# Kernel tuning notes

Hardware: AMD Instinct MI355X
Metric: run time of the kernel (lower is better)

The kernel has to match this reference:

```python
import jax, jax.numpy as jnp
import numpy as np

B, S, D, H = 2, 2048, 1024, 16
DK = D // H


def setup_inputs() -> dict:
    key = jax.random.key(0)
    ks = jax.random.split(key, 12)
    scale = 1.0 / np.sqrt(D)
    inp = {
        "query": jax.random.normal(ks[0], (B, S, D), jnp.float32),
        "key_in": jax.random.normal(ks[1], (B, S, D), jnp.float32),
        "value": jax.random.normal(ks[2], (B, S, D), jnp.float32),
        "mask": jnp.ones((1, 1, S, S), dtype=bool),
        "w_q": jax.random.normal(ks[3], (D, D), jnp.float32) * scale,
        "b_q": jnp.zeros((D,), jnp.float32),
        "w_k": jax.random.normal(ks[4], (D, D), jnp.float32) * scale,
        "b_k": jnp.zeros((D,), jnp.float32),
        "w_v": jax.random.normal(ks[5], (D, D), jnp.float32) * scale,
        "b_v": jnp.zeros((D,), jnp.float32),
        "w_o": jax.random.normal(ks[6], (D, D), jnp.float32) * scale,
        "b_o": jnp.zeros((D,), jnp.float32),
    }
    return inp


def reference(query, key_in, value, mask, w_q, b_q, w_k, b_k, w_v, b_v, w_o, b_o):
    # QKV projections (nn.Linear: x @ W.T + b; here weights stored as [D_in, D_out])
    q = query @ w_q + b_q          # [B, S, D]
    k = key_in @ w_k + b_k
    v = value @ w_v + b_v
    # split heads -> [B, H, S, DK]
    q = q.reshape(B, S, H, DK).transpose(0, 2, 1, 3)
    k = k.reshape(B, S, H, DK).transpose(0, 2, 1, 3)
    v = v.reshape(B, S, H, DK).transpose(0, 2, 1, 3)
    # scaled dot-product attention (naive: full [B,H,S,S] scores)
    scores = jnp.einsum('bhqd,bhkd->bhqk', q, k) / jnp.sqrt(jnp.float32(DK))
    scores = jnp.where(mask, scores, jnp.float32(-1e9))
    probs = jax.nn.softmax(scores, axis=-1)  # dropout p=0.0 -> identity
    x = jnp.einsum('bhqk,bhkd->bhqd', probs, v)  # [B, H, S, DK]
    x = x.transpose(0, 2, 1, 3).reshape(B, S, D)
    return x @ w_o + b_o
```

## Files before the change

### kernel.cpp

```cpp
#include <hip/hip_runtime.h>
#include <cstdint>
#include <cstddef>


typedef _Float16 f16_t;
typedef _Float16 f16x8 __attribute__((ext_vector_type(8)));
typedef _Float16 f16x4 __attribute__((ext_vector_type(4)));
typedef float    f32x4 __attribute__((ext_vector_type(4)));

#define S_LEN 2048
#define DMODEL 1024
#define NHEAD 16
#define DK 64
#define NKV (S_LEN / 64)

__device__ __forceinline__ void async_copy16(void* lds, const void* g) {
    __builtin_amdgcn_global_load_lds(
        (const __attribute__((address_space(1))) unsigned int*)g,
        (__attribute__((address_space(3))) unsigned int*)lds,
        16, 0, 0);
}

__device__ __forceinline__ float fexp2(float x) {
#if __has_builtin(__builtin_amdgcn_exp2f)
    return __builtin_amdgcn_exp2f(x);
#else
    return exp2f(x);
#endif
}

__global__ __launch_bounds__(256) void cvt3_kernel(
    const float* __restrict__ s0, const float* __restrict__ s1, const float* __restrict__ s2,
    f16_t* __restrict__ d0, f16_t* __restrict__ d1, f16_t* __restrict__ d2, int n)
{
    const float* s = blockIdx.y == 0 ? s0 : blockIdx.y == 1 ? s1 : s2;
    f16_t*       d = blockIdx.y == 0 ? d0 : blockIdx.y == 1 ? d1 : d2;
    int i = (blockIdx.x * 256 + threadIdx.x) * 4;
    if (i + 3 < n) {
        f32x4 v = *(const f32x4*)(s + i);
        f16x4 o;
        o[0] = (f16_t)v[0]; o[1] = (f16_t)v[1];
        o[2] = (f16_t)v[2]; o[3] = (f16_t)v[3];
        *(f16x4*)(d + i) = o;
    }
}

__global__ __launch_bounds__(256) void transpose_cvt_kernel(
    const float* __restrict__ w0, const float* __restrict__ w1,
    const float* __restrict__ w2, const float* __restrict__ w3,
    f16_t* __restrict__ wt_base)
{
    __shared__ float tile[32][33];
    int z = blockIdx.z;
    const float* w = z == 0 ? w0 : z == 1 ? w1 : z == 2 ? w2 : w3;
    f16_t* wt = wt_base + (size_t)z * DMODEL * DMODEL;
    int tx = threadIdx.x, ty = threadIdx.y;
    int bx = blockIdx.x * 32;
    int by = blockIdx.y * 32;
#pragma unroll
    for (int i = 0; i < 4; ++i)
        tile[ty + i * 8][tx] = w[(size_t)(bx + ty + i * 8) * DMODEL + by + tx];
    __syncthreads();
#pragma unroll
    for (int i = 0; i < 4; ++i)
        wt[(size_t)(by + ty + i * 8) * DMODEL + bx + tx] = (f16_t)tile[tx][ty + i * 8];
}

__global__ __launch_bounds__(256) void qkv_gemm_kernel(
    const f16_t* __restrict__ Aq, const f16_t* __restrict__ Ak, const f16_t* __restrict__ Av,
    const f16_t* __restrict__ Bt,
    const float* __restrict__ bq, const float* __restrict__ bk, const float* __restrict__ bv,
    f16_t* __restrict__ q_h, f16_t* __restrict__ k_h, f16_t* __restrict__ v_t)
{
    __shared__ f16_t As[128 * 32];
    __shared__ f16_t Bs[128 * 32];

    int tid  = threadIdx.x;
    int lane = tid & 63;
    int w    = tid >> 6;
    int wm   = w >> 1, wn = w & 1;

    int lin = blockIdx.y * 24 + blockIdx.x;
    int swz = (lin & 7) * 96 + (lin >> 3);
    int bx  = swz % 24, by = swz / 24;
    int row0 = by * 128;
    int col0 = bx * 128;
    int which = col0 >> 10;
    const f16_t* A = which == 0 ? Aq : which == 1 ? Ak : Av;
    const float* bias = which == 0 ? bq : which == 1 ? bk : bv;

    f32x4 acc[4][4] = {};

    for (int kk = 0; kk < 1024; kk += 32) {
        __syncthreads();
#pragma unroll
        for (int j = 0; j < 2; ++j) {
            int c = w * 2 + j;
            int r = c * 16 + (lane >> 2);
            int e = (lane & 3) * 8;
            async_copy16(&As[c * 512], A  + (size_t)(row0 + r) * 1024 + kk + e);
            async_copy16(&Bs[c * 512], Bt + (size_t)(col0 + r) * 1024 + kk + e);
        }
        __syncthreads();

        f16x8 a[4], b[4];
#pragma unroll
        for (int mi = 0; mi < 4; ++mi)
            a[mi] = *(const f16x8*)&As[(wm * 64 + mi * 16 + (lane & 15)) * 32 + (lane >> 4) * 8];
#pragma unroll
        for (int ni = 0; ni < 4; ++ni)
            b[ni] = *(const f16x8*)&Bs[(wn * 64 + ni * 16 + (lane & 15)) * 32 + (lane >> 4) * 8];
#pragma unroll
        for (int mi = 0; mi < 4; ++mi)
#pragma unroll
            for (int ni = 0; ni < 4; ++ni)
                acc[mi][ni] = __builtin_amdgcn_mfma_f32_16x16x32_f16(a[mi], b[ni], acc[mi][ni], 0, 0, 0);
    }

    const float QSCALE = 0.125f * 1.4426950408889634f;
#pragma unroll
    for (int mi = 0; mi < 4; ++mi) {
#pragma unroll
        for (int ni = 0; ni < 4; ++ni) {
#pragma unroll
            for (int r = 0; r < 4; ++r) {
                int grow = row0 + wm * 64 + mi * 16 + (lane >> 4) * 4 + r;
                int gcol = col0 + wn * 64 + ni * 16 + (lane & 15);
                int nc   = gcol & 1023;
                float v  = acc[mi][ni][r] + bias[nc];
                int bb = grow >> 11, ss = grow & 2047;
                int hh = nc >> 6,    dd = nc & 63;
                if (which == 0)
                    q_h[(((size_t)(bb * NHEAD + hh) * S_LEN + ss) << 6) + dd] = (f16_t)(v * QSCALE);
                else if (which == 1)
                    k_h[(((size_t)(bb * NHEAD + hh) * S_LEN + ss) << 6) + dd] = (f16_t)v;
                else
                    v_t[((size_t)(bb * NHEAD + hh) * DK + dd) * S_LEN + ss] = (f16_t)v;
            }
        }
    }
}

__global__ __launch_bounds__(256) void out_gemm_kernel(
    const f16_t* __restrict__ A, const f16_t* __restrict__ Bt,
    const float* __restrict__ bias, float* __restrict__ outp)
{
    __shared__ f16_t As[128 * 32];
    __shared__ f16_t Bs[128 * 32];

    int tid  = threadIdx.x;
    int lane = tid & 63;
    int w    = tid >> 6;
    int wm   = w >> 1, wn = w & 1;

    int lin = blockIdx.y * 8 + blockIdx.x;
    int swz = (lin & 7) * 32 + (lin >> 3);
    int row0 = (swz / 8) * 128;
    int col0 = (swz % 8) * 128;

    f32x4 acc[4][4] = {};

    for (int kk = 0; kk < 1024; kk += 32) {
        __syncthreads();
#pragma unroll
        for (int j = 0; j < 2; ++j) {
            int c = w * 2 + j;
            int r = c * 16 + (lane >> 2);
            int e = (lane & 3) * 8;
            async_copy16(&As[c * 512], A  + (size_t)(row0 + r) * 1024 + kk + e);
            async_copy16(&Bs[c * 512], Bt + (size_t)(col0 + r) * 1024 + kk + e);
        }
        __syncthreads();

        f16x8 a[4], b[4];
#pragma unroll
        for (int mi = 0; mi < 4; ++mi)
            a[mi] = *(const f16x8*)&As[(wm * 64 + mi * 16 + (lane & 15)) * 32 + (lane >> 4) * 8];
#pragma unroll
        for (int ni = 0; ni < 4; ++ni)
            b[ni] = *(const f16x8*)&Bs[(wn * 64 + ni * 16 + (lane & 15)) * 32 + (lane >> 4) * 8];
#pragma unroll
        for (int mi = 0; mi < 4; ++mi)
#pragma unroll
            for (int ni = 0; ni < 4; ++ni)
                acc[mi][ni] = __builtin_amdgcn_mfma_f32_16x16x32_f16(a[mi], b[ni], acc[mi][ni], 0, 0, 0);
    }

#pragma unroll
    for (int mi = 0; mi < 4; ++mi)
#pragma unroll
        for (int ni = 0; ni < 4; ++ni)
#pragma unroll
            for (int r = 0; r < 4; ++r) {
                int grow = row0 + wm * 64 + mi * 16 + (lane >> 4) * 4 + r;
                int gcol = col0 + wn * 64 + ni * 16 + (lane & 15);
                outp[(size_t)grow * 1024 + gcol] = acc[mi][ni][r] + bias[gcol];
            }
}

__global__ __launch_bounds__(256) void flash_kernel(
    const f16_t* __restrict__ Q, const f16_t* __restrict__ K,
    const f16_t* __restrict__ Vt, f16_t* __restrict__ Ao)
{
    __shared__ f16_t Kl[2][64 * 64];
    __shared__ f16_t Vl[64 * 64];
    __shared__ f16_t Pw[4][16 * 72];

    int tid  = threadIdx.x;
    int lane = tid & 63;
    int li   = lane & 15;
    int g    = lane >> 4;
    int w    = tid >> 6;

    int lin = blockIdx.y * 32 + blockIdx.x;
    int swz = (lin & 7) * 128 + (lin >> 3);
    int qt  = swz & 31;
    int bh  = swz >> 5;

    const size_t hbase = (size_t)bh * S_LEN * DK;
    const f16_t* Qh = Q  + hbase;
    const f16_t* Kh = K  + hbase;
    const f16_t* Vh = Vt + hbase;

    int q0 = qt * 64 + w * 16;

    f16x8 aq[2];
#pragma unroll
    for (int kc = 0; kc < 2; ++kc)
        aq[kc] = *(const f16x8*)(Qh + (size_t)(q0 + li) * DK + kc * 32 + g * 8);

    f32x4 ot[4] = {};
    float mrun = -1e30f;
    float lrun = 0.f;

    auto stageV = [&](int kt) {
#pragma unroll
        for (int j = 0; j < 2; ++j) {
            int r0  = w * 16 + j * 8;
            int row = r0 + (lane >> 3);
            int sl  = (lane & 7) ^ (row & 7);
            async_copy16(&Vl[r0 * 64], Vh + (size_t)row * S_LEN + kt * 64 + sl * 8);
        }
    };
    auto stageK = [&](int buf, int kt) {
#pragma unroll
        for (int j = 0; j < 2; ++j) {
            int r0  = w * 16 + j * 8;
            int row = r0 + (lane >> 3);
            int sl  = (lane & 7) ^ (row & 7);
            async_copy16(&Kl[buf][r0 * 64], Kh + (size_t)(kt * 64 + row) * 64 + sl * 8);
        }
    };

    stageK(0, 0);
    int cur = 0;

    for (int kt = 0; kt < NKV; ++kt) {
        __syncthreads();
        stageV(kt);
        if (kt + 1 < NKV) stageK(cur ^ 1, kt + 1);

        f32x4 s[4] = {};
        __builtin_amdgcn_s_setprio(1);
#pragma unroll
        for (int kc = 0; kc < 2; ++kc)
#pragma unroll
            for (int kn = 0; kn < 4; ++kn) {
                int row = kn * 16 + li;
                int sp  = (kc * 4 + g) ^ (row & 7);
                f16x8 ak = *(const f16x8*)&Kl[cur][row * 64 + sp * 8];
                s[kn] = __builtin_amdgcn_mfma_f32_16x16x32_f16(ak, aq[kc], s[kn], 0, 0, 0);
            }
        __builtin_amdgcn_s_setprio(0);

        {
            float mx = fmaxf(fmaxf(fmaxf(s[0][0], s[0][1]), fmaxf(s[0][2], s[0][3])),
                             fmaxf(fmaxf(s[1][0], s[1][1]), fmaxf(s[1][2], s[1][3])));
            mx = fmaxf(mx, fmaxf(fmaxf(fmaxf(s[2][0], s[2][1]), fmaxf(s[2][2], s[2][3])),
                                 fmaxf(fmaxf(s[3][0], s[3][1]), fmaxf(s[3][2], s[3][3]))));
            mx = fmaxf(mx, __shfl_xor(mx, 16));
            mx = fmaxf(mx, __shfl_xor(mx, 32));
            if (!__all(mx - mrun <= 8.0f)) {
                float mn = fmaxf(mrun, mx);
                float alpha = fexp2(mrun - mn);
                mrun = mn;
                lrun *= alpha;
#pragma unroll
                for (int nd = 0; nd < 4; ++nd)
#pragma unroll
                    for (int r = 0; r < 4; ++r)
                        ot[nd][r] *= alpha;
            }
            float rs = 0.f;
#pragma unroll
            for (int kn = 0; kn < 4; ++kn) {
                f16x4 pv;
#pragma unroll
                for (int r = 0; r < 4; ++r) {
                    float p = fexp2(s[kn][r] - mrun);
                    rs += p;
                    pv[r] = (f16_t)p;
                }
                *(f16x4*)&Pw[w][li * 72 + kn * 16 + g * 4] = pv;
            }
            rs += __shfl_xor(rs, 16);
            rs += __shfl_xor(rs, 32);
            lrun += rs;
        }

        if (kt + 1 < NKV) asm volatile("s_waitcnt vmcnt(2)" ::: "memory");
        else              asm volatile("s_waitcnt vmcnt(0)" ::: "memory");

        __builtin_amdgcn_s_setprio(1);
#pragma unroll
        for (int kc = 0; kc < 2; ++kc) {
            f16x8 bp = *(const f16x8*)&Pw[w][li * 72 + kc * 32 + g * 8];
#pragma unroll
            for (int nd = 0; nd < 4; ++nd) {
                int row = nd * 16 + li;
                int sp  = (kc * 4 + g) ^ (row & 7);
                f16x8 av = *(const f16x8*)&Vl[row * 64 + sp * 8];
                ot[nd] = __builtin_amdgcn_mfma_f32_16x16x32_f16(av, bp, ot[nd], 0, 0, 0);
            }
        }
        __builtin_amdgcn_s_setprio(0);

        cur ^= 1;
    }

    int b = bh >> 4, h = bh & 15;
    {
        float inv = 1.0f / lrun;
        int qrow = q0 + li;
        size_t base = (size_t)(b * S_LEN + qrow) * DMODEL + h * 64;
#pragma unroll
        for (int nd = 0; nd < 4; ++nd) {
            f16x4 ov;
#pragma unroll
            for (int r = 0; r < 4; ++r)
                ov[r] = (f16_t)(ot[nd][r] * inv);
            *(f16x4*)&Ao[base + nd * 16 + g * 4] = ov;
        }
    }
}

extern "C" void kernel_launch(void* const* d_in, const int* in_sizes, int n_in,
                              void* d_out, int out_size, void* d_ws, size_t ws_size,
                              hipStream_t stream)
{
    const float* query  = (const float*)d_in[0];
    const float* key_in = (const float*)d_in[1];
    const float* value  = (const float*)d_in[2];
    const float* w_q = (const float*)d_in[4];
    const float* b_q = (const float*)d_in[5];
    const float* w_k = (const float*)d_in[6];
    const float* b_k = (const float*)d_in[7];
    const float* w_v = (const float*)d_in[8];
    const float* b_v = (const float*)d_in[9];
    const float* w_o = (const float*)d_in[10];
    const float* b_o = (const float*)d_in[11];
    float* out = (float*)d_out;

    char* ws = (char*)d_ws;
    const size_t MB = 1024 * 1024;
    f16_t* x_q  = (f16_t*)(ws + 0 * MB);
    f16_t* x_k  = (f16_t*)(ws + 8 * MB);
    f16_t* x_v  = (f16_t*)(ws + 16 * MB);
    f16_t* wt   = (f16_t*)(ws + 24 * MB);
    f16_t* wt_o = (f16_t*)(ws + 30 * MB);
    f16_t* q_h  = (f16_t*)(ws + 32 * MB);
    f16_t* k_h  = (f16_t*)(ws + 40 * MB);
    f16_t* v_t  = (f16_t*)(ws + 48 * MB);
    f16_t* attn = (f16_t*)(ws + 56 * MB);

    const int n = 2 * S_LEN * DMODEL;

    cvt3_kernel<<<dim3(n / 1024, 3), 256, 0, stream>>>(query, key_in, value, x_q, x_k, x_v, n);
    transpose_cvt_kernel<<<dim3(32, 32, 4), dim3(32, 8), 0, stream>>>(w_q, w_k, w_v, w_o, wt);

    qkv_gemm_kernel<<<dim3(24, 32), 256, 0, stream>>>(
        x_q, x_k, x_v, wt, b_q, b_k, b_v, q_h, k_h, v_t);

    flash_kernel<<<dim3(32, 32), 256, 0, stream>>>(q_h, k_h, v_t, attn);

    out_gemm_kernel<<<dim3(8, 32), 256, 0, stream>>>(attn, wt_o, b_o, out);
}
```

Measured before the change: 152.3 us.

## Compute softmax row sums via MFMA with ones, hoist LDS/global address math

The attention kernel now computes the softmax denominator with an extra MFMA that multiplies a ones vector by the f16 probability tile, instead of scalar sums plus cross-lane shuffles. It also precomputes swizzled LDS offsets and global source pointers outside the KV loop, and packs probabilities with the cvt_pkrtz instruction. The goal is to cut VALU and shuffle work in the softmax step and address arithmetic in the inner loop. In exchange it adds MFMA work, sums the f16-rounded probabilities rather than the fp32 values, and uses round-toward-zero conversion.

```diff
diff --git a/kernel.cpp b/kernel.cpp
--- a/kernel.cpp
+++ b/kernel.cpp
@@ -7,6 +7,7 @@
 typedef _Float16 f16x8 __attribute__((ext_vector_type(8)));
 typedef _Float16 f16x4 __attribute__((ext_vector_type(4)));
 typedef float    f32x4 __attribute__((ext_vector_type(4)));
+typedef unsigned int u32x2 __attribute__((ext_vector_type(2)));
 
 #define S_LEN 2048
 #define DMODEL 1024
@@ -26,6 +27,15 @@
     return __builtin_amdgcn_exp2f(x);
 #else
     return exp2f(x);
+#endif
+}
+
+__device__ __forceinline__ unsigned int cvt_pk_u32(float a, float b) {
+#if __has_builtin(__builtin_amdgcn_cvt_pkrtz)
+    return __builtin_bit_cast(unsigned int, __builtin_amdgcn_cvt_pkrtz(a, b));
+#else
+    union { f16_t h[2]; unsigned int u; } r;
+    r.h[0] = (f16_t)a; r.h[1] = (f16_t)b; return r.u;
 #endif
 }
 
@@ -229,28 +239,33 @@
     for (int kc = 0; kc < 2; ++kc)
         aq[kc] = *(const f16x8*)(Qh + (size_t)(q0 + li) * DK + kc * 32 + g * 8);
 
+    f16x8 ones;
+#pragma unroll
+    for (int i = 0; i < 8; ++i) ones[i] = (f16_t)1.0f;
+
     f32x4 ot[4] = {};
+    f32x4 lacc = {};
     float mrun = -1e30f;
-    float lrun = 0.f;
+
+    int lr  = lane >> 3;
+    int sl8 = ((lane & 7) ^ lr) * 8;
+    const f16_t* srcK = Kh + (size_t)(w * 16 + lr) * 64    + sl8;
+    const f16_t* srcV = Vh + (size_t)(w * 16 + lr) * S_LEN + sl8;
 
     auto stageV = [&](int kt) {
-#pragma unroll
-        for (int j = 0; j < 2; ++j) {
-            int r0  = w * 16 + j * 8;
-            int row = r0 + (lane >> 3);
-            int sl  = (lane & 7) ^ (row & 7);
-            async_copy16(&Vl[r0 * 64], Vh + (size_t)row * S_LEN + kt * 64 + sl * 8);
-        }
+        async_copy16(&Vl[(w * 16) * 64],     srcV + kt * 64);
+        async_copy16(&Vl[(w * 16 + 8) * 64], srcV + 8 * S_LEN + kt * 64);
     };
     auto stageK = [&](int buf, int kt) {
-#pragma unroll
-        for (int j = 0; j < 2; ++j) {
-            int r0  = w * 16 + j * 8;
-            int row = r0 + (lane >> 3);
-            int sl  = (lane & 7) ^ (row & 7);
-            async_copy16(&Kl[buf][r0 * 64], Kh + (size_t)(kt * 64 + row) * 64 + sl * 8);
-        }
+        const f16_t* p = srcK + (size_t)kt * 4096;
+        async_copy16(&Kl[buf][(w * 16) * 64],     p);
+        async_copy16(&Kl[buf][(w * 16 + 8) * 64], p + 512);
     };
+
+    int x0 = li * 64 + ((g    ) ^ (li & 7)) * 8;
+    int x1 = li * 64 + ((4 + g) ^ (li & 7)) * 8;
+    int pww = li * 72 + g * 4;
+    int pwr = li * 72 + g * 8;
 
     stageK(0, 0);
     int cur = 0;
@@ -266,46 +281,41 @@
         for (int kc = 0; kc < 2; ++kc)
 #pragma unroll
             for (int kn = 0; kn < 4; ++kn) {
-                int row = kn * 16 + li;
-                int sp  = (kc * 4 + g) ^ (row & 7);
-                f16x8 ak = *(const f16x8*)&Kl[cur][row * 64 + sp * 8];
+                f16x8 ak = *(const f16x8*)&Kl[cur][kn * 1024 + (kc ? x1 : x0)];
                 s[kn] = __builtin_amdgcn_mfma_f32_16x16x32_f16(ak, aq[kc], s[kn], 0, 0, 0);
             }
         __builtin_amdgcn_s_setprio(0);
 
         {
-            float mx = fmaxf(fmaxf(fmaxf(s[0][0], s[0][1]), fmaxf(s[0][2], s[0][3])),
-                             fmaxf(fmaxf(s[1][0], s[1][1]), fmaxf(s[1][2], s[1][3])));
-            mx = fmaxf(mx, fmaxf(fmaxf(fmaxf(s[2][0], s[2][1]), fmaxf(s[2][2], s[2][3])),
-                                 fmaxf(fmaxf(s[3][0], s[3][1]), fmaxf(s[3][2], s[3][3]))));
+            float mx = fmaxf(s[0][0], s[0][1]);
+            mx = fmaxf(fmaxf(mx, s[0][2]), s[0][3]);
+            mx = fmaxf(fmaxf(mx, s[1][0]), s[1][1]);
+            mx = fmaxf(fmaxf(mx, s[1][2]), s[1][3]);
+            mx = fmaxf(fmaxf(mx, s[2][0]), s[2][1]);
+            mx = fmaxf(fmaxf(mx, s[2][2]), s[2][3]);
+            mx = fmaxf(fmaxf(mx, s[3][0]), s[3][1]);
+            mx = fmaxf(fmaxf(mx, s[3][2]), s[3][3]);
             mx = fmaxf(mx, __shfl_xor(mx, 16));
             mx = fmaxf(mx, __shfl_xor(mx, 32));
             if (!__all(mx - mrun <= 8.0f)) {
                 float mn = fmaxf(mrun, mx);
                 float alpha = fexp2(mrun - mn);
                 mrun = mn;
-                lrun *= alpha;
+#pragma unroll
+                for (int r = 0; r < 4; ++r) lacc[r] *= alpha;
 #pragma unroll
                 for (int nd = 0; nd < 4; ++nd)
 #pragma unroll
                     for (int r = 0; r < 4; ++r)
                         ot[nd][r] *= alpha;
             }
-            float rs = 0.f;
 #pragma unroll
             for (int kn = 0; kn < 4; ++kn) {
-                f16x4 pv;
-#pragma unroll
-                for (int r = 0; r < 4; ++r) {
-                    float p = fexp2(s[kn][r] - mrun);
-                    rs += p;
-                    pv[r] = (f16_t)p;
-                }
-                *(f16x4*)&Pw[w][li * 72 + kn * 16 + g * 4] = pv;
-            }
-            rs += __shfl_xor(rs, 16);
-            rs += __shfl_xor(rs, 32);
-            lrun += rs;
+                u32x2 pv;
+                pv[0] = cvt_pk_u32(fexp2(s[kn][0] - mrun), fexp2(s[kn][1] - mrun));
+                pv[1] = cvt_pk_u32(fexp2(s[kn][2] - mrun), fexp2(s[kn][3] - mrun));
+                *(u32x2*)&Pw[w][pww + kn * 16] = pv;
+            }
         }
 
         if (kt + 1 < NKV) asm volatile("s_waitcnt vmcnt(2)" ::: "memory");
@@ -314,12 +324,11 @@
         __builtin_amdgcn_s_setprio(1);
 #pragma unroll
         for (int kc = 0; kc < 2; ++kc) {
-            f16x8 bp = *(const f16x8*)&Pw[w][li * 72 + kc * 32 + g * 8];
+            f16x8 bp = *(const f16x8*)&Pw[w][pwr + kc * 32];
+            lacc = __builtin_amdgcn_mfma_f32_16x16x32_f16(ones, bp, lacc, 0, 0, 0);
 #pragma unroll
             for (int nd = 0; nd < 4; ++nd) {
-                int row = nd * 16 + li;
-                int sp  = (kc * 4 + g) ^ (row & 7);
-                f16x8 av = *(const f16x8*)&Vl[row * 64 + sp * 8];
+                f16x8 av = *(const f16x8*)&Vl[nd * 1024 + (kc ? x1 : x0)];
                 ot[nd] = __builtin_amdgcn_mfma_f32_16x16x32_f16(av, bp, ot[nd], 0, 0, 0);
             }
         }
@@ -330,7 +339,7 @@
 
     int b = bh >> 4, h = bh & 15;
     {
-        float inv = 1.0f / lrun;
+        float inv = 1.0f / lacc[0];
         int qrow = q0 + li;
         size_t base = (size_t)(b * S_LEN + qrow) * DMODEL + h * 64;
 #pragma unroll
```

Measured after the change: 146.8 us. -3.6%, faster.
